# Optimization experiments

Hardware: AMD Instinct MI355X
Metric: run time of the kernel (lower is better)

The kernel has to match this reference:

```python
import jax, jax.numpy as jnp
import numpy as np

GROUPS = 2
EPS = 1e-5


def channel_shuffle(x, groups=2):
    b, c, h, w = x.shape
    x = x.reshape(b, groups, c // groups, h, w)
    x = jnp.transpose(x, (0, 2, 1, 3, 4))
    return x.reshape(b, c, h, w)


def binarize_weight(w):
    # w: (O, I/g, k, k). scaling_factor = mean |w| over (in,kh,kw), detached.
    scale = jax.lax.stop_gradient(jnp.mean(jnp.abs(w), axis=(1, 2, 3), keepdims=True))
    bw = scale * jnp.sign(w)
    cl = jnp.clip(w, -1.0, 1.0)
    # STE: forward value = bw, gradient flows through clamp
    return jax.lax.stop_gradient(bw) - jax.lax.stop_gradient(cl) + cl


@jax.custom_vjp
def bin_act(x):
    return jnp.sign(x)


def _bin_act_fwd(x):
    return jnp.sign(x), x


def _bin_act_bwd(x, g):
    scale = jnp.where((x >= 1.0) | (x <= -1.0), 0.01, 1.0)
    return (g * scale,)


bin_act.defvjp(_bin_act_fwd, _bin_act_bwd)


def grouped_bin_conv(x, w, pad):
    return jax.lax.conv_general_dilated(
        x, binarize_weight(w), window_strides=(1, 1),
        padding=[(pad, pad), (pad, pad)],
        dimension_numbers=('NCHW', 'OIHW', 'NCHW'),
        feature_group_count=GROUPS)


def batchnorm(x, gamma, beta):
    # training-mode BN: biased batch statistics over (N,H,W)
    mu = jnp.mean(x, axis=(0, 2, 3), keepdims=True)
    var = jnp.mean((x - mu) ** 2, axis=(0, 2, 3), keepdims=True)
    xn = (x - mu) * jax.lax.rsqrt(var + EPS)
    return xn * gamma[None, :, None, None] + beta[None, :, None, None]


def add_bias(x, b):
    return x + b[None, :, None, None]


def prelu(x, a):
    return jnp.where(x >= 0, x, a[None, :, None, None] * x)


def setup_inputs() -> dict:
    key = jax.random.key(0)
    ks = jax.random.split(key, 4)
    C, half = 256, 128
    x = jax.random.normal(ks[0], (32, C, 56, 56), dtype=jnp.float32)
    # two BinaryConvs (64,128,3,3) stacked -> grouped (128,128,3,3)
    w3 = jax.random.uniform(ks[1], (half, C // GROUPS, 3, 3), dtype=jnp.float32) * 0.001
    w1 = jax.random.uniform(ks[2], (half, C // GROUPS, 1, 1), dtype=jnp.float32) * 0.001
    z = jnp.zeros((C,), jnp.float32)
    return {
        'x': x, 'w3': w3, 'w1': w1,
        'b1': z, 'g1': jnp.ones((half,), jnp.float32), 'be1': jnp.zeros((half,), jnp.float32),
        'b2_1': z, 'a2': jnp.full((C,), 0.25, jnp.float32), 'b2_2': z,
        'b3_1': z, 'g3': jnp.ones((half,), jnp.float32), 'be3': jnp.zeros((half,), jnp.float32),
        'b4_1': z, 'a4': jnp.full((C,), 0.25, jnp.float32), 'b4_2': z,
    }


def reference(x, w3, w1, b1, g1, be1, b2_1, a2, b2_2, b3_1, g3, be3, b4_1, a4, b4_2):
    half = w3.shape[0]  # out_channel // 2 = 128
    x = channel_shuffle(x, GROUPS)
    x1 = bin_act(add_bias(x, b1))
    x1 = batchnorm(grouped_bin_conv(x1, w3, pad=1), g1, be1)
    x1_res = x[:, half:]
    x1 = x1 + x[:, :half]
    x2 = jnp.concatenate([x1, x1_res], axis=1)
    x2 = add_bias(prelu(add_bias(x2, b2_1), a2), b2_2)
    x2 = add_bias(x2, b3_1)
    x3 = bin_act(x2)
    x3 = batchnorm(grouped_bin_conv(x3, w1, pad=0), g3, be3)
    x3_res = x2[:, half:]
    x3 = x3 + x2[:, :half]
    x4 = jnp.concatenate([x3, x3_res], axis=1)
    x5 = add_bias(prelu(add_bias(x4, b4_1), a4), b4_2)
    return x5
```

## Files before the change

### kernel.cpp

```cpp
#include <hip/hip_runtime.h>
#include <stdint.h>

typedef unsigned short ushort_t;
typedef unsigned int uint_t;
typedef _Float16 half_t;

#define B_N 32
#define C_N 256
#define HALF_N 128
#define H_N 56
#define W_N 56
#define HW_N 3136
#define NPIX (B_N * HW_N)
#define EPS_D 1e-5
#define W3S 40
#define PWS 16

__global__ void prep_kernel(const float* __restrict__ w3, const float* __restrict__ w1,
                            uint_t* __restrict__ wbits3, uint_t* __restrict__ wbits1,
                            uint_t* __restrict__ popcw3,
                            double* __restrict__ scale3, double* __restrict__ scale1,
                            double* __restrict__ sums1, double* __restrict__ sums2,
                            uint_t* __restrict__ oflags) {
    __shared__ double red[128];
    __shared__ int ipw[2][9];
    __shared__ int flsh[2];
    int t = threadIdx.x;
    int blk = blockIdx.x;
    int lane = t & 63;
    int wv = t >> 6;
    if (blk == 0) {
        sums1[t] = 0.0; sums1[128 + t] = 0.0;
        sums2[t] = 0.0; sums2[128 + t] = 0.0;
    }
    if (blk < 128) {
        int o = blk;
        double acc = 0.0;
        int anynp = 0;
        #pragma unroll
        for (int j = 0; j < 9; ++j) {
            float v = w3[o * 1152 + t * 9 + j];
            acc += fabs((double)v);
            anynp |= (v <= 0.f) ? 1 : 0;
            unsigned long long b = __ballot(v > 0.f);
            if (lane == 0) {
                wbits3[o * W3S + j * 4 + wv * 2 + 0] = (uint_t)b;
                wbits3[o * W3S + j * 4 + wv * 2 + 1] = (uint_t)(b >> 32);
                ipw[wv][j] = __popcll(b);
            }
        }
        unsigned long long m = __ballot(anynp != 0);
        if (lane == 0) flsh[wv] = (m != 0ull) ? 1 : 0;
        red[t] = acc; __syncthreads();
        for (int s = 64; s > 0; s >>= 1) { if (t < s) red[t] += red[t + s]; __syncthreads(); }
        if (t == 0) { scale3[o] = red[0] / 1152.0; oflags[o] = (uint_t)(flsh[0] | flsh[1]); }
        if (t < 9) popcw3[o * PWS + t] = (uint_t)(ipw[0][t] + ipw[1][t]);
    } else {
        int o = blk - 128;
        float v = w1[o * 128 + t];
        unsigned long long b = __ballot(v > 0.f);
        unsigned long long m = __ballot(v <= 0.f);
        if (lane == 0) {
            wbits1[o * 8 + wv * 2 + 0] = (uint_t)b;
            wbits1[o * 8 + wv * 2 + 1] = (uint_t)(b >> 32);
            flsh[wv] = (m != 0ull) ? 1 : 0;
        }
        red[t] = fabs((double)v); __syncthreads();
        for (int s = 64; s > 0; s >>= 1) { if (t < s) red[t] += red[t + s]; __syncthreads(); }
        if (t == 0) { scale1[o] = red[0] / 128.0; oflags[128 + o] = (uint_t)(flsh[0] | flsh[1]); }
    }
}

__global__ __launch_bounds__(256) void sign1_kernel(const float* __restrict__ x,
                                                    const float* __restrict__ b1,
                                                    uint_t* __restrict__ vb,
                                                    const uint_t* __restrict__ oflags,
                                                    uint_t* __restrict__ fin) {
    __shared__ int fl[4];
    int t = threadIdx.x;
    if (blockIdx.x == 0 && blockIdx.y == 0) {
        int lane = t & 63, wv4 = t >> 6;
        uint_t f = oflags[t];
        unsigned long long m = __ballot(f != 0u);
        if (lane == 0) fl[wv4] = (m != 0ull) ? 1 : 0;
        __syncthreads();
        if (t == 0) { fin[0] = (uint_t)(fl[0] | fl[1]); fin[1] = (uint_t)(fl[2] | fl[3]); }
    }
    int p = blockIdx.x * 256 + t;
    int cb = blockIdx.y * 64;
    int b = p / HW_N;
    int hw = p - b * HW_N;
    const float* xb = x + (size_t)b * C_N * HW_N + hw;
    #pragma unroll
    for (int wq = 0; wq < 2; ++wq) {
        uint_t bits = 0u;
        #pragma unroll
        for (int j = 0; j < 32; ++j) {
            int c = cb + wq * 32 + j;
            int src = ((c & 1) << 7) + (c >> 1);
            double v = (double)xb[(size_t)src * HW_N] + (double)b1[c];
            bits |= (v > 0.0) ? (1u << j) : 0u;
        }
        vb[(size_t)((cb >> 5) + wq) * NPIX + p] = bits;
    }
}

__global__ __launch_bounds__(256) void conv3_kernel(const uint_t* __restrict__ vb,
                                                    const uint_t* __restrict__ wbits3,
                                                    const uint_t* __restrict__ popcw3,
                                                    half_t* __restrict__ yh,
                                                    double* __restrict__ sums,
                                                    const uint_t* __restrict__ fin) {
    __shared__ short dlds[32][258];
    __shared__ int partS[8][32];
    __shared__ int partS2[8][32];
    int t = threadIdx.x;
    int lane = t & 63;
    int wv = t >> 6;
    bool fast = (fin[0] == 0u);
    int yb = blockIdx.y;
    if (fast && (yb & 1)) return;
    int g = yb >> 1;
    int oh = yb & 1;
    int o0 = g * 64 + oh * 32;
    int p = blockIdx.x * 256 + t;
    int hw = p % HW_N;
    int h = hw / W_N;
    int w = hw - h * W_N;
    const uint_t* vbase = vb + (size_t)g * 4 * NPIX;

    uint_t v[9][4];
    int inv[9];
    int nvalid = 0;
    #pragma unroll
    for (int j = 0; j < 9; ++j) {
        int kh = j / 3 - 1, kw = j - (j / 3) * 3 - 1;
        int hh = h + kh, ww = w + kw;
        bool valid = (hh >= 0) && (hh < H_N) && (ww >= 0) && (ww < W_N);
        inv[j] = valid ? 0 : 1;
        nvalid += valid ? 1 : 0;
        int off = p + kh * W_N + kw;
        #pragma unroll
        for (int q = 0; q < 4; ++q)
            v[j][q] = valid ? vbase[(size_t)q * NPIX + off] : 0u;
    }
    int base = 128 * nvalid;

    if (fast) {
        int P = 0;
        #pragma unroll
        for (int j = 0; j < 9; ++j)
            #pragma unroll
            for (int q = 0; q < 4; ++q)
                P += __popc(v[j][q]);
        int dot = 2 * P - base;
        yh[(size_t)o0 * NPIX + p] = (half_t)(float)dot;
        int s = dot, s2 = dot * dot;
        #pragma unroll
        for (int off = 32; off > 0; off >>= 1) {
            s  += __shfl_xor(s, off);
            s2 += __shfl_xor(s2, off);
        }
        if (lane == 0) { partS[0][wv] = s; partS2[0][wv] = s2; }
        __syncthreads();
        if (t == 0) {
            partS[1][0]  = partS[0][0] + partS[0][1] + partS[0][2] + partS[0][3];
            partS2[1][0] = partS2[0][0] + partS2[0][1] + partS2[0][2] + partS2[0][3];
        }
        __syncthreads();
        if (t < 64) {
            atomicAdd(&sums[o0 + t], (double)partS[1][0]);
            atomicAdd(&sums[128 + o0 + t], (double)partS2[1][0]);
        }
        return;
    }

    half_t* yrow = yh + (size_t)o0 * NPIX + p;
    for (int oi = 0; oi < 32; ++oi) {
        const uint_t* wo = wbits3 + (size_t)(o0 + oi) * W3S;
        const uint_t* pw = popcw3 + (size_t)(o0 + oi) * PWS;
        int acc = 0;
        #pragma unroll
        for (int j = 0; j < 9; ++j)
            #pragma unroll
            for (int q = 0; q < 4; ++q)
                acc += __popc(v[j][q] ^ wo[j * 4 + q]);
        int corr = 0;
        #pragma unroll
        for (int j = 0; j < 9; ++j) corr += inv[j] * (int)pw[j];
        int dot = base - 2 * (acc - corr);
        yrow[(size_t)oi * NPIX] = (half_t)(float)dot;
        dlds[oi][t] = (short)dot;
    }
    __syncthreads();
    {
        int o = t & 31, seg = t >> 5;
        const int* r32 = (const int*)(&dlds[o][seg * 32]);
        int S = 0, S2 = 0;
        #pragma unroll
        for (int j = 0; j < 16; ++j) {
            int pr = r32[j];
            int d0 = (int)(short)(pr & 0xffff);
            int d1 = pr >> 16;
            S += d0 + d1; S2 += d0 * d0 + d1 * d1;
        }
        partS[seg][o] = S; partS2[seg][o] = S2;
    }
    __syncthreads();
    if (t < 32) {
        int S = 0, S2 = 0;
        #pragma unroll
        for (int s8 = 0; s8 < 8; ++s8) { S += partS[s8][t]; S2 += partS2[s8][t]; }
        int c = o0 + t;
        atomicAdd(&sums[c], (double)S);
        atomicAdd(&sums[128 + c], (double)S2);
    }
}

__device__ __forceinline__ void coef_entry(const double* __restrict__ sums,
                                           const double* __restrict__ scale,
                                           const float* __restrict__ gamma,
                                           const float* __restrict__ beta,
                                           int c, double* coefL) {
    double M = (double)NPIX;
    double mean = sums[c] / M;
    double var = sums[128 + c] / M - mean * mean;
    double s = scale[c];
    double r = 1.0 / sqrt(s * s * var + EPS_D);
    double g = (double)gamma[c];
    coefL[c] = s * r * g;
    coefL[128 + c] = (double)beta[c] - s * mean * r * g;
}

__device__ __forceinline__ void coef_entry_f(const double* __restrict__ sums,
                                             const double* __restrict__ scale,
                                             const float* __restrict__ gamma,
                                             const float* __restrict__ beta,
                                             int c, float* cf) {
    double M = (double)NPIX;
    double mean = sums[c] / M;
    double var = sums[128 + c] / M - mean * mean;
    double s = scale[c];
    double r = 1.0 / sqrt(s * s * var + EPS_D);
    double g = (double)gamma[c];
    cf[c] = (float)(s * r * g);
    cf[128 + c] = (float)((double)beta[c] - s * mean * r * g);
}

__device__ __forceinline__ double x2_val(double xs, double K, bool hasy,
                                         const double* coef1, int c,
                                         const float* __restrict__ b2_1, const float* __restrict__ a2,
                                         const float* __restrict__ b2_2, const float* __restrict__ b3_1) {
    int ci = c & 127;
    double t = hasy ? (coef1[ci] * K + coef1[128 + ci] + xs) : xs;
    t += (double)b2_1[c];
    double a = (double)a2[c];
    t = (t >= 0.0) ? t : a * t;
    t += (double)b2_2[c];
    t += (double)b3_1[c];
    return t;
}

__global__ __launch_bounds__(256) void x2c1_kernel(
        const float* __restrict__ x, const half_t* __restrict__ y1h,
        const double* __restrict__ sums1, const double* __restrict__ scale3,
        const float* __restrict__ g1, const float* __restrict__ be1,
        const float* __restrict__ b2_1, const float* __restrict__ a2,
        const float* __restrict__ b2_2, const float* __restrict__ b3_1,
        const uint_t* __restrict__ wbits1,
        half_t* __restrict__ y3h, double* __restrict__ sums2,
        const uint_t* __restrict__ fin) {
    __shared__ double coefL[256];
    __shared__ short dst[32][258];
    __shared__ int partS[8][32];
    __shared__ int partS2[8][32];
    int t = threadIdx.x;
    int lane = t & 63;
    int wv = t >> 6;
    int g = blockIdx.y;
    bool fast3 = (fin[0] == 0u);
    bool fast1 = (fin[1] == 0u);
    if (g == 0 && t < 128) coef_entry(sums1, scale3, g1, be1, t, coefL);
    __syncthreads();

    int p = blockIdx.x * 256 + t;
    int b = p / HW_N;
    int hw = p - b * HW_N;
    const float* xb = x + (size_t)b * C_N * HW_N + hw;
    int c0 = g * 128;

    uint_t w0_, w1_, w2_, w3_;
    if (g == 0) {
        if (fast3) {
            double K0  = (double)(float)y1h[p];
            double K64 = (double)(float)y1h[(size_t)64 * NPIX + p];
            #pragma unroll
            for (int wq = 0; wq < 4; ++wq) {
                uint_t bits = 0u;
                double Kc = (wq < 2) ? K0 : K64;
                #pragma unroll
                for (int j = 0; j < 32; ++j) {
                    int c = wq * 32 + j;
                    int src = ((c & 1) << 7) + (c >> 1);
                    double xs = (double)xb[(size_t)src * HW_N];
                    double v = x2_val(xs, Kc, true, coefL, c, b2_1, a2, b2_2, b3_1);
                    bits |= (v > 0.0) ? (1u << j) : 0u;
                }
                if (wq == 0) w0_ = bits; else if (wq == 1) w1_ = bits;
                else if (wq == 2) w2_ = bits; else w3_ = bits;
            }
        } else {
            #pragma unroll
            for (int wq = 0; wq < 4; ++wq) {
                uint_t bits = 0u;
                #pragma unroll
                for (int j = 0; j < 32; ++j) {
                    int c = wq * 32 + j;
                    int src = ((c & 1) << 7) + (c >> 1);
                    double xs = (double)xb[(size_t)src * HW_N];
                    double K = (double)(float)y1h[(size_t)c * NPIX + p];
                    double v = x2_val(xs, K, true, coefL, c, b2_1, a2, b2_2, b3_1);
                    bits |= (v > 0.0) ? (1u << j) : 0u;
                }
                if (wq == 0) w0_ = bits; else if (wq == 1) w1_ = bits;
                else if (wq == 2) w2_ = bits; else w3_ = bits;
            }
        }
    } else {
        #pragma unroll
        for (int wq = 0; wq < 4; ++wq) {
            uint_t bits = 0u;
            #pragma unroll
            for (int j = 0; j < 32; ++j) {
                int c = c0 + wq * 32 + j;
                int src = ((c & 1) << 7) + (c >> 1);
                double xs = (double)xb[(size_t)src * HW_N];
                double v = x2_val(xs, 0.0, false, coefL, c, b2_1, a2, b2_2, b3_1);
                bits |= (v > 0.0) ? (1u << j) : 0u;
            }
            if (wq == 0) w0_ = bits; else if (wq == 1) w1_ = bits;
            else if (wq == 2) w2_ = bits; else w3_ = bits;
        }
    }

    int obase = g * 64;
    if (fast1) {
        int P = __popc(w0_) + __popc(w1_) + __popc(w2_) + __popc(w3_);
        int dotv = 2 * P - 128;
        y3h[(size_t)obase * NPIX + p] = (half_t)(float)dotv;
        int s = dotv, s2 = dotv * dotv;
        #pragma unroll
        for (int off = 32; off > 0; off >>= 1) {
            s  += __shfl_xor(s, off);
            s2 += __shfl_xor(s2, off);
        }
        if (lane == 0) { partS[0][wv] = s; partS2[0][wv] = s2; }
        __syncthreads();
        if (t == 0) {
            partS[1][0]  = partS[0][0] + partS[0][1] + partS[0][2] + partS[0][3];
            partS2[1][0] = partS2[0][0] + partS2[0][1] + partS2[0][2] + partS2[0][3];
        }
        __syncthreads();
        if (t < 64) {
            atomicAdd(&sums2[obase + t], (double)partS[1][0]);
            atomicAdd(&sums2[128 + obase + t], (double)partS2[1][0]);
        }
        return;
    }

    #pragma unroll
    for (int ch = 0; ch < 2; ++ch) {
        #pragma unroll
        for (int oi = 0; oi < 32; ++oi) {
            int o = obase + ch * 32 + oi;
            const uint_t* wo = wbits1 + (size_t)o * 8;
            int acc = __popc(w0_ ^ wo[0]) + __popc(w1_ ^ wo[1])
                    + __popc(w2_ ^ wo[2]) + __popc(w3_ ^ wo[3]);
            int dot = 128 - 2 * acc;
            y3h[(size_t)o * NPIX + p] = (half_t)(float)dot;
            dst[oi][t] = (short)dot;
        }
        __syncthreads();
        {
            int o = t & 31, seg = t >> 5;
            const int* r32 = (const int*)(&dst[o][seg * 32]);
            int S = 0, S2 = 0;
            #pragma unroll
            for (int j = 0; j < 16; ++j) {
                int pr = r32[j];
                int d0 = (int)(short)(pr & 0xffff);
                int d1 = pr >> 16;
                S += d0 + d1; S2 += d0 * d0 + d1 * d1;
            }
            partS[seg][o] = S; partS2[seg][o] = S2;
        }
        __syncthreads();
        if (t < 32) {
            int S = 0, S2 = 0;
            #pragma unroll
            for (int s8 = 0; s8 < 8; ++s8) { S += partS[s8][t]; S2 += partS2[s8][t]; }
            int c = obase + ch * 32 + t;
            atomicAdd(&sums2[c], (double)S);
            atomicAdd(&sums2[128 + c], (double)S2);
        }
        __syncthreads();
    }
}

__global__ __launch_bounds__(256) void out_kernel(
        const float* __restrict__ x, const half_t* __restrict__ y1h,
        const half_t* __restrict__ y3h,
        const double* __restrict__ sums1, const double* __restrict__ scale3,
        const float* __restrict__ g1, const float* __restrict__ be1,
        const double* __restrict__ sums2, const double* __restrict__ scale1,
        const float* __restrict__ g3, const float* __restrict__ be3,
        const float* __restrict__ b2_1, const float* __restrict__ a2,
        const float* __restrict__ b2_2, const float* __restrict__ b3_1,
        const float* __restrict__ b4_1, const float* __restrict__ a4,
        const float* __restrict__ b4_2, float* __restrict__ out,
        const uint_t* __restrict__ fin) {
    __shared__ float c1f[256];
    __shared__ float c3f[256];
    int t = threadIdx.x;
    if (t < 128) coef_entry_f(sums1, scale3, g1, be1, t, c1f);
    else coef_entry_f(sums2, scale1, g3, be3, t - 128, c3f);
    __syncthreads();
    int c = blockIdx.y;
    bool h1 = (c < 128);
    int src = ((c & 1) << 7) + (c >> 1);
    int ci = c & 127;
    int y1slice = (fin[0] == 0u) ? ((ci < 64) ? 0 : 64) : ci;
    int y3slice = (fin[1] == 0u) ? ((ci < 64) ? 0 : 64) : ci;
    float b21 = b2_1[c], aa2v = a2[c], b23 = b2_2[c] + b3_1[c];
    float b41 = b4_1[c], aa4v = a4[c], b42 = b4_2[c];
    float c1 = c1f[ci], c1b = c1f[128 + ci];
    float c3 = c3f[ci], c3b = c3f[128 + ci];
    const half_t* y1p = y1h + (size_t)y1slice * NPIX;
    const half_t* y3p = y3h + (size_t)y3slice * NPIX;
    #pragma unroll
    for (int i = 0; i < 8; ++i) {
        int p = blockIdx.x * 2048 + i * 256 + t;
        int b = p / HW_N;
        int hw = p - b * HW_N;
        float xs = x[((size_t)b * C_N + src) * HW_N + hw];
        float v = h1 ? fmaf(c1, (float)y1p[p], c1b) + xs : xs;
        v += b21;
        v = (v >= 0.f) ? v : aa2v * v;
        v += b23;
        float t2 = v;
        if (h1) v = fmaf(c3, (float)y3p[p], c3b) + t2;
        v += b41;
        v = (v >= 0.f) ? v : aa4v * v;
        v += b42;
        out[((size_t)b * C_N + c) * HW_N + hw] = v;
    }
}

extern "C" void kernel_launch(void* const* d_in, const int* in_sizes, int n_in,
                              void* d_out, int out_size, void* d_ws, size_t ws_size,
                              hipStream_t stream) {
    const float* x    = (const float*)d_in[0];
    const float* w3   = (const float*)d_in[1];
    const float* w1   = (const float*)d_in[2];
    const float* b1   = (const float*)d_in[3];
    const float* g1   = (const float*)d_in[4];
    const float* be1  = (const float*)d_in[5];
    const float* b2_1 = (const float*)d_in[6];
    const float* a2   = (const float*)d_in[7];
    const float* b2_2 = (const float*)d_in[8];
    const float* b3_1 = (const float*)d_in[9];
    const float* g3   = (const float*)d_in[10];
    const float* be3  = (const float*)d_in[11];
    const float* b4_1 = (const float*)d_in[12];
    const float* a4   = (const float*)d_in[13];
    const float* b4_2 = (const float*)d_in[14];

    char* ws = (char*)d_ws;
    half_t* y1h    = (half_t*)(ws + 0);
    half_t* y3h    = (half_t*)(ws + 25690112);
    uint_t* wbits3 = (uint_t*)(ws + 51380224);
    uint_t* wbits1 = (uint_t*)(ws + 51400704);
    uint_t* popcw3 = (uint_t*)(ws + 51404800);
    double* scale3 = (double*)(ws + 51412992);
    double* scale1 = (double*)(ws + 51414016);
    double* sums1  = (double*)(ws + 51415040);
    double* sums2  = (double*)(ws + 51417088);
    uint_t* oflags = (uint_t*)(ws + 51419136);
    uint_t* fin    = (uint_t*)(ws + 51420160);

    uint_t* vb1 = (uint_t*)((char*)d_out + 0);
    float*  outp = (float*)d_out;

    prep_kernel<<<256, 128, 0, stream>>>(w3, w1, wbits3, wbits1, popcw3,
                                         scale3, scale1, sums1, sums2, oflags);
    sign1_kernel<<<dim3(NPIX / 256, 4), 256, 0, stream>>>(x, b1, vb1, oflags, fin);
    conv3_kernel<<<dim3(NPIX / 256, 4), 256, 0, stream>>>(vb1, wbits3, popcw3, y1h, sums1, fin);
    x2c1_kernel<<<dim3(NPIX / 256, 2), 256, 0, stream>>>(x, y1h, sums1, scale3, g1, be1,
                                                         b2_1, a2, b2_2, b3_1,
                                                         wbits1, y3h, sums2, fin);
    out_kernel<<<dim3(NPIX / 2048, 256), 256, 0, stream>>>(x, y1h, y3h,
                                                           sums1, scale3, g1, be1,
                                                           sums2, scale1, g3, be3,
                                                           b2_1, a2, b2_2, b3_1,
                                                           b4_1, a4, b4_2, outp, fin);
}
```

Measured before the change: 280.2 us.

## Vectorize pixel loads and fuse residual-half output into x2c1 kernel

Sign1, x2c1 and out kernels now each handle 2-4 consecutive pixels per thread using float2/float4 and half2/half4 vector loads and stores. The upper 128 channels, which do not depend on either convolution, are now finished and written directly inside x2c1 while x is already loaded. This lets out_kernel launch over only the lower 128 channels and avoids re-reading x for half the output. The aim is fewer memory transactions and less duplicated traffic. In exchange, threads hold more registers and x2c1 writes output with a channel-strided pattern.

```diff
diff --git a/kernel.cpp b/kernel.cpp
--- a/kernel.cpp
+++ b/kernel.cpp
@@ -4,6 +4,12 @@
 typedef unsigned short ushort_t;
 typedef unsigned int uint_t;
 typedef _Float16 half_t;
+
+typedef float  float4_t __attribute__((ext_vector_type(4)));
+typedef float  float2_t __attribute__((ext_vector_type(2)));
+typedef _Float16 half4_t __attribute__((ext_vector_type(4)));
+typedef _Float16 half2_t __attribute__((ext_vector_type(2)));
+typedef uint_t uint4_t  __attribute__((ext_vector_type(4)));
 
 #define B_N 32
 #define C_N 256
@@ -86,23 +92,25 @@
         __syncthreads();
         if (t == 0) { fin[0] = (uint_t)(fl[0] | fl[1]); fin[1] = (uint_t)(fl[2] | fl[3]); }
     }
-    int p = blockIdx.x * 256 + t;
-    int cb = blockIdx.y * 64;
+    int p = blockIdx.x * 1024 + t * 4;
+    int cb = blockIdx.y * 32;
     int b = p / HW_N;
     int hw = p - b * HW_N;
     const float* xb = x + (size_t)b * C_N * HW_N + hw;
+    uint_t w0 = 0, w1 = 0, w2 = 0, w3 = 0;
     #pragma unroll
-    for (int wq = 0; wq < 2; ++wq) {
-        uint_t bits = 0u;
-        #pragma unroll
-        for (int j = 0; j < 32; ++j) {
-            int c = cb + wq * 32 + j;
-            int src = ((c & 1) << 7) + (c >> 1);
-            double v = (double)xb[(size_t)src * HW_N] + (double)b1[c];
-            bits |= (v > 0.0) ? (1u << j) : 0u;
-        }
-        vb[(size_t)((cb >> 5) + wq) * NPIX + p] = bits;
-    }
+    for (int j = 0; j < 32; ++j) {
+        int c = cb + j;
+        int src = ((c & 1) << 7) + (c >> 1);
+        float4_t xv = *(const float4_t*)(xb + (size_t)src * HW_N);
+        double bc = (double)b1[c];
+        if ((double)xv[0] + bc > 0.0) w0 |= (1u << j);
+        if ((double)xv[1] + bc > 0.0) w1 |= (1u << j);
+        if ((double)xv[2] + bc > 0.0) w2 |= (1u << j);
+        if ((double)xv[3] + bc > 0.0) w3 |= (1u << j);
+    }
+    uint4_t o4; o4[0] = w0; o4[1] = w1; o4[2] = w2; o4[3] = w3;
+    *(uint4_t*)(vb + (size_t)(cb >> 5) * NPIX + p) = o4;
 }
 
 __global__ __launch_bounds__(256) void conv3_kernel(const uint_t* __restrict__ vb,
@@ -261,7 +269,7 @@
     return t;
 }
 
-__global__ __launch_bounds__(256) void x2c1_kernel(
+__global__ __launch_bounds__(128) void x2c1_kernel(
         const float* __restrict__ x, const half_t* __restrict__ y1h,
         const double* __restrict__ sums1, const double* __restrict__ scale3,
         const float* __restrict__ g1, const float* __restrict__ be1,
@@ -269,86 +277,108 @@
         const float* __restrict__ b2_2, const float* __restrict__ b3_1,
         const uint_t* __restrict__ wbits1,
         half_t* __restrict__ y3h, double* __restrict__ sums2,
+        const float* __restrict__ b4_1, const float* __restrict__ a4,
+        const float* __restrict__ b4_2, float* __restrict__ out,
         const uint_t* __restrict__ fin) {
     __shared__ double coefL[256];
     __shared__ short dst[32][258];
-    __shared__ int partS[8][32];
-    __shared__ int partS2[8][32];
+    __shared__ int partS[4][32];
+    __shared__ int partS2[4][32];
     int t = threadIdx.x;
     int lane = t & 63;
     int wv = t >> 6;
     int g = blockIdx.y;
     bool fast3 = (fin[0] == 0u);
     bool fast1 = (fin[1] == 0u);
-    if (g == 0 && t < 128) coef_entry(sums1, scale3, g1, be1, t, coefL);
+    if (g == 0) coef_entry(sums1, scale3, g1, be1, t, coefL);
     __syncthreads();
 
-    int p = blockIdx.x * 256 + t;
+    int p = blockIdx.x * 256 + t * 2;
     int b = p / HW_N;
     int hw = p - b * HW_N;
     const float* xb = x + (size_t)b * C_N * HW_N + hw;
-    int c0 = g * 128;
-
-    uint_t w0_, w1_, w2_, w3_;
+
+    uint_t q0 = 0, q1 = 0, q2 = 0, q3 = 0;
+    uint_t r0 = 0, r1 = 0, r2 = 0, r3 = 0;
     if (g == 0) {
         if (fast3) {
-            double K0  = (double)(float)y1h[p];
-            double K64 = (double)(float)y1h[(size_t)64 * NPIX + p];
+            half2_t k0  = *(const half2_t*)(y1h + p);
+            half2_t k64 = *(const half2_t*)(y1h + (size_t)64 * NPIX + p);
+            double K0a = (double)(float)k0[0],  K0b = (double)(float)k0[1];
+            double K6a = (double)(float)k64[0], K6b = (double)(float)k64[1];
             #pragma unroll
             for (int wq = 0; wq < 4; ++wq) {
-                uint_t bits = 0u;
-                double Kc = (wq < 2) ? K0 : K64;
+                uint_t ba = 0, bb = 0;
+                double Ka = (wq < 2) ? K0a : K6a;
+                double Kb = (wq < 2) ? K0b : K6b;
                 #pragma unroll
                 for (int j = 0; j < 32; ++j) {
                     int c = wq * 32 + j;
                     int src = ((c & 1) << 7) + (c >> 1);
-                    double xs = (double)xb[(size_t)src * HW_N];
-                    double v = x2_val(xs, Kc, true, coefL, c, b2_1, a2, b2_2, b3_1);
-                    bits |= (v > 0.0) ? (1u << j) : 0u;
+                    float2_t xv = *(const float2_t*)(xb + (size_t)src * HW_N);
+                    double va = x2_val((double)xv[0], Ka, true, coefL, c, b2_1, a2, b2_2, b3_1);
+                    double vb_ = x2_val((double)xv[1], Kb, true, coefL, c, b2_1, a2, b2_2, b3_1);
+                    ba |= (va > 0.0) ? (1u << j) : 0u;
+                    bb |= (vb_ > 0.0) ? (1u << j) : 0u;
                 }
-                if (wq == 0) w0_ = bits; else if (wq == 1) w1_ = bits;
-                else if (wq == 2) w2_ = bits; else w3_ = bits;
+                if (wq == 0) { q0 = ba; r0 = bb; } else if (wq == 1) { q1 = ba; r1 = bb; }
+                else if (wq == 2) { q2 = ba; r2 = bb; } else { q3 = ba; r3 = bb; }
             }
         } else {
             #pragma unroll
             for (int wq = 0; wq < 4; ++wq) {
-                uint_t bits = 0u;
+                uint_t ba = 0, bb = 0;
                 #pragma unroll
                 for (int j = 0; j < 32; ++j) {
                     int c = wq * 32 + j;
                     int src = ((c & 1) << 7) + (c >> 1);
-                    double xs = (double)xb[(size_t)src * HW_N];
-                    double K = (double)(float)y1h[(size_t)c * NPIX + p];
-                    double v = x2_val(xs, K, true, coefL, c, b2_1, a2, b2_2, b3_1);
-                    bits |= (v > 0.0) ? (1u << j) : 0u;
+                    float2_t xv = *(const float2_t*)(xb + (size_t)src * HW_N);
+                    half2_t kv = *(const half2_t*)(y1h + (size_t)c * NPIX + p);
+                    double va = x2_val((double)xv[0], (double)(float)kv[0], true, coefL, c, b2_1, a2, b2_2, b3_1);
+                    double vb_ = x2_val((double)xv[1], (double)(float)kv[1], true, coefL, c, b2_1, a2, b2_2, b3_1);
+                    ba |= (va > 0.0) ? (1u << j) : 0u;
+                    bb |= (vb_ > 0.0) ? (1u << j) : 0u;
                 }
-                if (wq == 0) w0_ = bits; else if (wq == 1) w1_ = bits;
-                else if (wq == 2) w2_ = bits; else w3_ = bits;
+                if (wq == 0) { q0 = ba; r0 = bb; } else if (wq == 1) { q1 = ba; r1 = bb; }
+                else if (wq == 2) { q2 = ba; r2 = bb; } else { q3 = ba; r3 = bb; }
             }
         }
     } else {
         #pragma unroll
         for (int wq = 0; wq < 4; ++wq) {
-            uint_t bits = 0u;
+            uint_t ba = 0, bb = 0;
             #pragma unroll
             for (int j = 0; j < 32; ++j) {
-                int c = c0 + wq * 32 + j;
+                int c = 128 + wq * 32 + j;
                 int src = ((c & 1) << 7) + (c >> 1);
-                double xs = (double)xb[(size_t)src * HW_N];
-                double v = x2_val(xs, 0.0, false, coefL, c, b2_1, a2, b2_2, b3_1);
-                bits |= (v > 0.0) ? (1u << j) : 0u;
+                float2_t xv = *(const float2_t*)(xb + (size_t)src * HW_N);
+                double va = x2_val((double)xv[0], 0.0, false, coefL, c, b2_1, a2, b2_2, b3_1);
+                double vb_ = x2_val((double)xv[1], 0.0, false, coefL, c, b2_1, a2, b2_2, b3_1);
+                ba |= (va > 0.0) ? (1u << j) : 0u;
+                bb |= (vb_ > 0.0) ? (1u << j) : 0u;
+                float b41c = b4_1[c], a4c = a4[c], b42c = b4_2[c];
+                float f0 = (float)va + b41c;
+                f0 = (f0 >= 0.f) ? f0 : a4c * f0;
+                f0 += b42c;
+                float f1 = (float)vb_ + b41c;
+                f1 = (f1 >= 0.f) ? f1 : a4c * f1;
+                f1 += b42c;
+                float2_t ov; ov[0] = f0; ov[1] = f1;
+                *(float2_t*)(out + ((size_t)b * C_N + c) * HW_N + hw) = ov;
             }
-            if (wq == 0) w0_ = bits; else if (wq == 1) w1_ = bits;
-            else if (wq == 2) w2_ = bits; else w3_ = bits;
+            if (wq == 0) { q0 = ba; r0 = bb; } else if (wq == 1) { q1 = ba; r1 = bb; }
+            else if (wq == 2) { q2 = ba; r2 = bb; } else { q3 = ba; r3 = bb; }
         }
     }
 
     int obase = g * 64;
     if (fast1) {
-        int P = __popc(w0_) + __popc(w1_) + __popc(w2_) + __popc(w3_);
-        int dotv = 2 * P - 128;
-        y3h[(size_t)obase * NPIX + p] = (half_t)(float)dotv;
-        int s = dotv, s2 = dotv * dotv;
+        int P0 = __popc(q0) + __popc(q1) + __popc(q2) + __popc(q3);
+        int P1 = __popc(r0) + __popc(r1) + __popc(r2) + __popc(r3);
+        int d0 = 2 * P0 - 128, d1 = 2 * P1 - 128;
+        half2_t yv; yv[0] = (half_t)(float)d0; yv[1] = (half_t)(float)d1;
+        *(half2_t*)(y3h + (size_t)obase * NPIX + p) = yv;
+        int s = d0 + d1, s2 = d0 * d0 + d1 * d1;
         #pragma unroll
         for (int off = 32; off > 0; off >>= 1) {
             s  += __shfl_xor(s, off);
@@ -357,8 +387,8 @@
         if (lane == 0) { partS[0][wv] = s; partS2[0][wv] = s2; }
         __syncthreads();
         if (t == 0) {
-            partS[1][0]  = partS[0][0] + partS[0][1] + partS[0][2] + partS[0][3];
-            partS2[1][0] = partS2[0][0] + partS2[0][1] + partS2[0][2] + partS2[0][3];
+            partS[1][0]  = partS[0][0] + partS[0][1];
+            partS2[1][0] = partS2[0][0] + partS2[0][1];
         }
         __syncthreads();
         if (t < 64) {
@@ -374,31 +404,33 @@
         for (int oi = 0; oi < 32; ++oi) {
             int o = obase + ch * 32 + oi;
             const uint_t* wo = wbits1 + (size_t)o * 8;
-            int acc = __popc(w0_ ^ wo[0]) + __popc(w1_ ^ wo[1])
-                    + __popc(w2_ ^ wo[2]) + __popc(w3_ ^ wo[3]);
-            int dot = 128 - 2 * acc;
-            y3h[(size_t)o * NPIX + p] = (half_t)(float)dot;
-            dst[oi][t] = (short)dot;
+            int a0 = __popc(q0 ^ wo[0]) + __popc(q1 ^ wo[1])
+                   + __popc(q2 ^ wo[2]) + __popc(q3 ^ wo[3]);
+            int a1 = __popc(r0 ^ wo[0]) + __popc(r1 ^ wo[1])
+                   + __popc(r2 ^ wo[2]) + __popc(r3 ^ wo[3]);
+            int d0 = 128 - 2 * a0, d1 = 128 - 2 * a1;
+            half2_t yv; yv[0] = (half_t)(float)d0; yv[1] = (half_t)(float)d1;
+            *(half2_t*)(y3h + (size_t)o * NPIX + p) = yv;
+            *(int*)&dst[oi][t * 2] = (d0 & 0xffff) | (d1 << 16);
         }
         __syncthreads();
         {
             int o = t & 31, seg = t >> 5;
-            const int* r32 = (const int*)(&dst[o][seg * 32]);
+            const int* r32 = (const int*)(&dst[o][seg * 64]);
             int S = 0, S2 = 0;
             #pragma unroll
-            for (int j = 0; j < 16; ++j) {
+            for (int j = 0; j < 32; ++j) {
                 int pr = r32[j];
-                int d0 = (int)(short)(pr & 0xffff);
-                int d1 = pr >> 16;
-                S += d0 + d1; S2 += d0 * d0 + d1 * d1;
+                int e0 = (int)(short)(pr & 0xffff);
+                int e1 = pr >> 16;
+                S += e0 + e1; S2 += e0 * e0 + e1 * e1;
             }
             partS[seg][o] = S; partS2[seg][o] = S2;
         }
         __syncthreads();
         if (t < 32) {
-            int S = 0, S2 = 0;
-            #pragma unroll
-            for (int s8 = 0; s8 < 8; ++s8) { S += partS[s8][t]; S2 += partS2[s8][t]; }
+            int S  = partS[0][t] + partS[1][t] + partS[2][t] + partS[3][t];
+            int S2 = partS2[0][t] + partS2[1][t] + partS2[2][t] + partS2[3][t];
             int c = obase + ch * 32 + t;
             atomicAdd(&sums2[c], (double)S);
             atomicAdd(&sums2[128 + c], (double)S2);
@@ -426,33 +458,38 @@
     else coef_entry_f(sums2, scale1, g3, be3, t - 128, c3f);
     __syncthreads();
     int c = blockIdx.y;
-    bool h1 = (c < 128);
     int src = ((c & 1) << 7) + (c >> 1);
-    int ci = c & 127;
-    int y1slice = (fin[0] == 0u) ? ((ci < 64) ? 0 : 64) : ci;
-    int y3slice = (fin[1] == 0u) ? ((ci < 64) ? 0 : 64) : ci;
+    int y1slice = (fin[0] == 0u) ? ((c < 64) ? 0 : 64) : c;
+    int y3slice = (fin[1] == 0u) ? ((c < 64) ? 0 : 64) : c;
     float b21 = b2_1[c], aa2v = a2[c], b23 = b2_2[c] + b3_1[c];
     float b41 = b4_1[c], aa4v = a4[c], b42 = b4_2[c];
-    float c1 = c1f[ci], c1b = c1f[128 + ci];
-    float c3 = c3f[ci], c3b = c3f[128 + ci];
+    float c1 = c1f[c], c1b = c1f[128 + c];
+    float c3 = c3f[c], c3b = c3f[128 + c];
     const half_t* y1p = y1h + (size_t)y1slice * NPIX;
     const half_t* y3p = y3h + (size_t)y3slice * NPIX;
     #pragma unroll
-    for (int i = 0; i < 8; ++i) {
-        int p = blockIdx.x * 2048 + i * 256 + t;
+    for (int i = 0; i < 2; ++i) {
+        int p = blockIdx.x * 2048 + i * 1024 + t * 4;
         int b = p / HW_N;
         int hw = p - b * HW_N;
-        float xs = x[((size_t)b * C_N + src) * HW_N + hw];
-        float v = h1 ? fmaf(c1, (float)y1p[p], c1b) + xs : xs;
-        v += b21;
-        v = (v >= 0.f) ? v : aa2v * v;
-        v += b23;
-        float t2 = v;
-        if (h1) v = fmaf(c3, (float)y3p[p], c3b) + t2;
-        v += b41;
-        v = (v >= 0.f) ? v : aa4v * v;
-        v += b42;
-        out[((size_t)b * C_N + c) * HW_N + hw] = v;
+        float4_t xs = *(const float4_t*)(x + ((size_t)b * C_N + src) * HW_N + hw);
+        half4_t y1v = *(const half4_t*)(y1p + p);
+        half4_t y3v = *(const half4_t*)(y3p + p);
+        float4_t ov;
+        #pragma unroll
+        for (int k = 0; k < 4; ++k) {
+            float v = fmaf(c1, (float)y1v[k], c1b) + xs[k];
+            v += b21;
+            v = (v >= 0.f) ? v : aa2v * v;
+            v += b23;
+            float t2 = v;
+            v = fmaf(c3, (float)y3v[k], c3b) + t2;
+            v += b41;
+            v = (v >= 0.f) ? v : aa4v * v;
+            v += b42;
+            ov[k] = v;
+        }
+        *(float4_t*)(out + ((size_t)b * C_N + c) * HW_N + hw) = ov;
     }
 }
 
@@ -493,12 +530,13 @@
 
     prep_kernel<<<256, 128, 0, stream>>>(w3, w1, wbits3, wbits1, popcw3,
                                          scale3, scale1, sums1, sums2, oflags);
-    sign1_kernel<<<dim3(NPIX / 256, 4), 256, 0, stream>>>(x, b1, vb1, oflags, fin);
+    sign1_kernel<<<dim3(NPIX / 1024, 8), 256, 0, stream>>>(x, b1, vb1, oflags, fin);
     conv3_kernel<<<dim3(NPIX / 256, 4), 256, 0, stream>>>(vb1, wbits3, popcw3, y1h, sums1, fin);
-    x2c1_kernel<<<dim3(NPIX / 256, 2), 256, 0, stream>>>(x, y1h, sums1, scale3, g1, be1,
+    x2c1_kernel<<<dim3(NPIX / 256, 2), 128, 0, stream>>>(x, y1h, sums1, scale3, g1, be1,
                                                          b2_1, a2, b2_2, b3_1,
-                                                         wbits1, y3h, sums2, fin);
-    out_kernel<<<dim3(NPIX / 2048, 256), 256, 0, stream>>>(x, y1h, y3h,
+                                                         wbits1, y3h, sums2,
+                                                         b4_1, a4, b4_2, outp, fin);
+    out_kernel<<<dim3(NPIX / 2048, 128), 256, 0, stream>>>(x, y1h, y3h,
                                                            sums1, scale3, g1, be1,
                                                            sums2, scale1, g3, be3,
                                                            b2_1, a2, b2_2, b3_1,
```

After: 288.0 us. 1.03x slower.
